# Performance work log

Hardware: AMD Instinct MI355X
Metric: run time of the kernel (lower is better)

## Reference

```python
import jax, jax.numpy as jnp
import numpy as np

B, M, L, D = 64, 128, 20, 1024


def setup_inputs() -> dict:
    key = jax.random.key(0)
    ks = jax.random.split(key, 16)
    s = 0.05  # weight scale to keep LSTM gates out of saturation
    rn = lambda k, shape: jax.random.normal(k, shape, jnp.float32) * s
    return {
        'encoder_out': jax.random.normal(ks[0], (B, M + 1, D), jnp.float32),
        'obj_seq': jax.random.randint(ks[1], (B, L), 0, M),
        'att_mask': jnp.ones((B, M + 1), jnp.int32),
        'bos_w': rn(ks[2], (1, D)),
        'eos_w': rn(ks[3], (1, D)),
        'Wp': rn(ks[4], (D, D)), 'bp': jnp.zeros((D,), jnp.float32),
        'Wih1': rn(ks[5], (4 * D, 3 * D)), 'Whh1': rn(ks[6], (4 * D, D)),
        'bih1': jnp.zeros((4 * D,), jnp.float32), 'bhh1': jnp.zeros((4 * D,), jnp.float32),
        'Wih2': rn(ks[7], (4 * D, 2 * D)), 'Whh2': rn(ks[8], (4 * D, D)),
        'bih2': jnp.zeros((4 * D,), jnp.float32), 'bhh2': jnp.zeros((4 * D,), jnp.float32),
        'Wah': rn(ks[9], (D, D)), 'bah': jnp.zeros((D,), jnp.float32),
        'wa': rn(ks[10], (D,)), 'ba': jnp.zeros((1,), jnp.float32),
        'Wae': rn(ks[11], (D, D)), 'bae': jnp.zeros((D,), jnp.float32),
        'Woe': rn(ks[12], (D, D)), 'boe': jnp.zeros((D,), jnp.float32),
    }


def _lstm_cell(x, h, c, Wih, Whh, bih, bhh):
    # torch LSTMCell gate order: i, f, g, o
    g = x @ Wih.T + bih + h @ Whh.T + bhh
    i, f, gg, o = jnp.split(g, 4, axis=-1)
    c_new = jax.nn.sigmoid(f) * c + jax.nn.sigmoid(i) * jnp.tanh(gg)
    h_new = jax.nn.sigmoid(o) * jnp.tanh(c_new)
    return h_new, c_new


def _forward(encoder_out, obj_seq, att_mask, bos_w, eos_w, Wp, bp,
             Wih1, Whh1, bih1, bhh1, Wih2, Whh2, bih2, bhh2,
             Wah, bah, wa, ba, Wae, bae, Woe, boe):
    b, _, d = encoder_out.shape
    gv = encoder_out[:, 0, :]                      # [B, D]
    att_feats = encoder_out[:, 1:, :]              # [B, M, D]
    idx = jnp.broadcast_to(obj_seq[:, :, None], obj_seq.shape + (d,)).astype(jnp.int32)
    obj_feat = jnp.take_along_axis(att_feats, idx, axis=1)          # [B, L, D]
    bos = jnp.broadcast_to(bos_w, (b, 1, d))
    obj_feat = jnp.concatenate([bos, obj_feat], axis=1)             # [B, L+1, D]
    p_att = att_feats @ Wp.T + bp                  # [B, M, D]
    amask = att_mask[:, 1:]                        # [B, M]

    def attend(h1):
        dot = jnp.tanh(p_att + (h1 @ Wah.T + bah)[:, None, :])      # [B, M, D]
        score = dot @ wa + ba[0]                                    # [B, M]
        score = jnp.where(amask == 0, -1e9, score)
        alpha = jax.nn.softmax(score, axis=-1)
        return jnp.einsum('bm,bmd->bd', alpha, att_feats)

    def step(carry, x_t):
        h1, c1, h2, c2 = carry
        inp1 = jnp.concatenate([h2, gv, x_t], axis=-1)              # [B, 3D]
        h1, c1 = _lstm_cell(inp1, h1, c1, Wih1, Whh1, bih1, bhh1)
        att = attend(h1)
        inp2 = jnp.concatenate([att, h1], axis=-1)                  # [B, 2D]
        h2, c2 = _lstm_cell(inp2, h2, c2, Wih2, Whh2, bih2, bhh2)
        return (h1, c1, h2, c2), h2

    z = jnp.zeros((b, d), encoder_out.dtype)
    _, outs = jax.lax.scan(step, (z, z, z, z), jnp.swapaxes(obj_feat, 0, 1))
    outputs = jnp.swapaxes(outs, 0, 1)             # [B, L+1, D]

    # NCE branch (cfg.LOSSES.NCE.STOP_GRAD = True)
    nce_att = jax.lax.stop_gradient(att_feats)
    afe = nce_att @ Wae.T + bae
    eos = jnp.broadcast_to(eos_w, (b, 1, d))
    afe = jnp.concatenate([eos, afe], axis=1)      # [B, M+1, D]
    ofe = outputs @ Woe.T + boe                    # [B, L+1, D]
    nce_logit = jnp.einsum('bld,bmd->blm', ofe, afe)  # [B, L+1, M+1]
    return outputs, nce_logit


def reference(encoder_out, obj_seq, att_mask, bos_w, eos_w, Wp, bp,
              Wih1, Whh1, bih1, bhh1, Wih2, Whh2, bih2, bhh2,
              Wah, bah, wa, ba, Wae, bae, Woe, boe):
    return _forward(encoder_out, obj_seq, att_mask, bos_w, eos_w, Wp, bp,
                    Wih1, Whh1, bih1, bhh1, Wih2, Whh2, bih2, bhh2,
                    Wah, bah, wa, ba, Wae, bae, Woe, boe)
```

## Files before the change

kernel.cpp:

```cpp
#include <hip/hip_runtime.h>
#include <cmath>

typedef unsigned short u16;
typedef __attribute__((ext_vector_type(8))) short short8;
typedef __attribute__((ext_vector_type(4))) float floatx4;
typedef __attribute__((address_space(3))) unsigned int lds_u32;
typedef const __attribute__((address_space(1))) unsigned int glob_u32;

__device__ __forceinline__ u16 f2bf(float f) {
    unsigned u = __float_as_uint(f);
    unsigned r = u + 0x7fffu + ((u >> 16) & 1u);
    return (u16)(r >> 16);
}
__device__ __forceinline__ float bf2f(u16 h) { return __uint_as_float(((unsigned)h) << 16); }
__device__ __forceinline__ void split2(float x, u16& hi, u16& lo) {
    hi = f2bf(x);
    lo = f2bf(x - bf2f(hi));
}
__device__ __forceinline__ float sigm(float x) {
    x = fminf(fmaxf(x, -30.f), 30.f);
    return 1.0f / (1.0f + __expf(-x));
}
__device__ __forceinline__ float ftanh(float x) {
    x = fminf(fmaxf(x, -15.f), 15.f);
    float e = __expf(2.f * x);
    return (e - 1.f) / (e + 1.f);
}
__device__ __forceinline__ void gload16(const void* g, void* l) {
    __builtin_amdgcn_global_load_lds((glob_u32*)g, (lds_u32*)l, 16, 0, 0);
}

__global__ __launch_bounds__(256) void k_cvt(const float* __restrict__ s, u16* __restrict__ d, int n4) {
    int i = blockIdx.x * 256 + threadIdx.x;
    int stride = gridDim.x * 256;
    for (; i < n4; i += stride) {
        float4 v = ((const float4*)s)[i];
        ushort4 o;
        o.x = f2bf(v.x); o.y = f2bf(v.y); o.z = f2bf(v.z); o.w = f2bf(v.w);
        ((ushort4*)d)[i] = o;
    }
}

__global__ __launch_bounds__(256) void k_cvt_att(const float* __restrict__ enc, u16* __restrict__ dst) {
    int m = blockIdx.x, b = blockIdx.y, tid = threadIdx.x;
    const float* src = enc + ((size_t)b * 129 + 1 + m) * 1024;
    float4 v = *(const float4*)(src + tid * 4);
    ushort4 o;
    o.x = f2bf(v.x); o.y = f2bf(v.y); o.z = f2bf(v.z); o.w = f2bf(v.w);
    *(ushort4*)(dst + ((size_t)b * 128 + m) * 1024 + tid * 4) = o;
}

__global__ __launch_bounds__(256) void k_splitp(const float* __restrict__ s, u16* __restrict__ hi,
                                                u16* __restrict__ lo, int n4) {
    int i = blockIdx.x * 256 + threadIdx.x;
    int stride = gridDim.x * 256;
    for (; i < n4; i += stride) {
        float4 v = ((const float4*)s)[i];
        ushort4 h, l;
        split2(v.x, h.x, l.x); split2(v.y, h.y, l.y);
        split2(v.z, h.z, l.z); split2(v.w, h.w, l.w);
        ((ushort4*)hi)[i] = h;
        ((ushort4*)lo)[i] = l;
    }
}

__global__ __launch_bounds__(256) void k_build_w1cat_i(const float* __restrict__ Wih1, const float* __restrict__ Whh1,
                                                       u16* __restrict__ dh, u16* __restrict__ dl) {
    int r = blockIdx.x;
    int srcrow = (r & 3) * 1024 + (r >> 2);
    int c = threadIdx.x * 8;
    const float* src = (c < 1024) ? (Wih1 + (size_t)srcrow * 3072 + c) : (Whh1 + (size_t)srcrow * 1024 + (c - 1024));
    short8 h, l;
#pragma unroll
    for (int j = 0; j < 8; ++j) { u16 hh, ll; split2(src[j], hh, ll); h[j] = (short)hh; l[j] = (short)ll; }
    *(short8*)(dh + (size_t)r * 2048 + c) = h;
    *(short8*)(dl + (size_t)r * 2048 + c) = l;
}

__global__ __launch_bounds__(384) void k_build_wcat2_i(const float* __restrict__ Wih2, const float* __restrict__ Whh2,
                                                       u16* __restrict__ dh, u16* __restrict__ dl) {
    int r = blockIdx.x;
    int srcrow = (r & 3) * 1024 + (r >> 2);
    int c = threadIdx.x * 8;
    const float* src = (c < 2048) ? (Wih2 + (size_t)srcrow * 2048 + c) : (Whh2 + (size_t)srcrow * 1024 + (c - 2048));
    short8 h, l;
#pragma unroll
    for (int j = 0; j < 8; ++j) { u16 hh, ll; split2(src[j], hh, ll); h[j] = (short)hh; l[j] = (short)ll; }
    *(short8*)(dh + (size_t)r * 3072 + c) = h;
    *(short8*)(dl + (size_t)r * 3072 + c) = l;
}

__global__ __launch_bounds__(256) void k_build_wx1_i(const float* __restrict__ Wih1, u16* __restrict__ dh,
                                                     u16* __restrict__ dl) {
    int r = blockIdx.x;
    int srcrow = (r & 3) * 1024 + (r >> 2);
    int c = threadIdx.x * 8;
    const float* src = Wih1 + (size_t)srcrow * 3072 + 1024 + c;
    short8 h, l;
#pragma unroll
    for (int j = 0; j < 8; ++j) { u16 hh, ll; split2(src[j], hh, ll); h[j] = (short)hh; l[j] = (short)ll; }
    *(short8*)(dh + (size_t)r * 2048 + c) = h;
    *(short8*)(dl + (size_t)r * 2048 + c) = l;
}

__global__ __launch_bounds__(256) void k_mkbias(const float* __restrict__ s1, const float* __restrict__ s2,
                                                float* __restrict__ dst) {
    int r = blockIdx.x * 256 + threadIdx.x;
    int srcn = (r & 3) * 1024 + (r >> 2);
    dst[r] = s1[srcn] + s2[srcn];
}

__global__ __launch_bounds__(256) void k_build_xaug(const float* __restrict__ enc, const int* __restrict__ obj,
                                                    const float* __restrict__ bos_w, u16* __restrict__ dh,
                                                    u16* __restrict__ dl) {
    int b = blockIdx.x, t = blockIdx.y, tid = threadIdx.x;
    const float* gv = enc + (size_t)b * 129 * 1024;
    const float* xr;
    if (t == 0) xr = bos_w;
    else {
        int idx = obj[b * 20 + (t - 1)];
        idx = min(max(idx, 0), 127);
        xr = enc + ((size_t)b * 129 + 1 + idx) * 1024;
    }
    size_t rowoff = ((size_t)b * 21 + t) * 2048;
    float4 v0 = *(const float4*)(gv + tid * 4);
    float4 v1 = *(const float4*)(xr + tid * 4);
    ushort4 h0, l0, h1, l1;
    split2(v0.x, h0.x, l0.x); split2(v0.y, h0.y, l0.y); split2(v0.z, h0.z, l0.z); split2(v0.w, h0.w, l0.w);
    split2(v1.x, h1.x, l1.x); split2(v1.y, h1.y, l1.y); split2(v1.z, h1.z, l1.z); split2(v1.w, h1.w, l1.w);
    *(ushort4*)(dh + rowoff + tid * 4) = h0;
    *(ushort4*)(dl + rowoff + tid * 4) = l0;
    *(ushort4*)(dh + rowoff + 1024 + tid * 4) = h1;
    *(ushort4*)(dl + rowoff + 1024 + tid * 4) = l1;
}

template <int APASS, int BPASS, int AREMAP, bool BF16OUT>
__global__ __launch_bounds__(256)
void k_gemm3(const u16* __restrict__ Ah, const u16* __restrict__ Al, int lda,
             const u16* __restrict__ Wh, const u16* __restrict__ Wl, int ldw,
             const float* __restrict__ b1, const float* __restrict__ b2,
             void* __restrict__ Cout, int ldc, int Mrows, int K) {
    constexpr int NP = APASS + BPASS;
    __shared__ char lds[2][NP][8192];
    const int tid = threadIdx.x;
    const int lane = tid & 63;
    const int lr = lane & 15, lk = lane >> 4;
    const int m0 = blockIdx.y * 128, n0 = blockIdx.x * 128;
    const int wid = tid >> 6;
    const int wr = wid >> 1, wc = wid & 1;
    const int wbyte = (tid & 192) * 16;

    floatx4 acc[4][4] = {};
    const int nt = K >> 5;

    auto stage = [&](int bb, int kt) {
        int k0 = kt * 32;
#pragma unroll
        for (int i = 0; i < 2; ++i) {
            int p = i * 256 + tid;
            int s = p ^ ((p >> 2) & 3);
            int row = s >> 2, kc = s & 3;
            size_t aoff;
            int gm = m0 + row;
            if (AREMAP == 1) aoff = (((size_t)(gm >> 7)) * 129 + 1 + (gm & 127)) * 1024 + k0 + kc * 8;
            else {
                int cm = gm < Mrows ? gm : Mrows - 1;
                aoff = (size_t)cm * lda + k0 + kc * 8;
            }
            gload16(Ah + aoff, &lds[bb][0][i * 4096 + wbyte]);
            if constexpr (APASS == 2) gload16(Al + aoff, &lds[bb][1][i * 4096 + wbyte]);
            size_t woff = (size_t)(n0 + row) * ldw + k0 + kc * 8;
            gload16(Wh + woff, &lds[bb][APASS][i * 4096 + wbyte]);
            if constexpr (BPASS == 2) gload16(Wl + woff, &lds[bb][APASS + 1][i * 4096 + wbyte]);
        }
    };

    stage(0, 0);
    __syncthreads();
    for (int t = 0; t < nt; ++t) {
        int bb = t & 1;
        if (t + 1 < nt) stage(bb ^ 1, t + 1);
        short8 ah_[4], al_[4], bh_[4], bl_[4];
#pragma unroll
        for (int mi = 0; mi < 4; ++mi) {
            int row = wr * 64 + mi * 16 + lr;
            int slot = (row * 4 + (lk ^ (row & 3))) * 16;
            ah_[mi] = *(const short8*)&lds[bb][0][slot];
            if constexpr (APASS == 2) al_[mi] = *(const short8*)&lds[bb][1][slot];
        }
#pragma unroll
        for (int ni = 0; ni < 4; ++ni) {
            int row = wc * 64 + ni * 16 + lr;
            int slot = (row * 4 + (lk ^ (row & 3))) * 16;
            bh_[ni] = *(const short8*)&lds[bb][APASS][slot];
            if constexpr (BPASS == 2) bl_[ni] = *(const short8*)&lds[bb][APASS + 1][slot];
        }
#pragma unroll
        for (int mi = 0; mi < 4; ++mi)
#pragma unroll
            for (int ni = 0; ni < 4; ++ni) {
                acc[mi][ni] = __builtin_amdgcn_mfma_f32_16x16x32_bf16(ah_[mi], bh_[ni], acc[mi][ni], 0, 0, 0);
                if constexpr (BPASS == 2)
                    acc[mi][ni] = __builtin_amdgcn_mfma_f32_16x16x32_bf16(ah_[mi], bl_[ni], acc[mi][ni], 0, 0, 0);
                if constexpr (APASS == 2)
                    acc[mi][ni] = __builtin_amdgcn_mfma_f32_16x16x32_bf16(al_[mi], bh_[ni], acc[mi][ni], 0, 0, 0);
            }
        __syncthreads();
    }
#pragma unroll
    for (int mi = 0; mi < 4; ++mi) {
#pragma unroll
        for (int r = 0; r < 4; ++r) {
            int gm = m0 + wr * 64 + mi * 16 + lk * 4 + r;
            if (AREMAP == 0 && gm >= Mrows) continue;
#pragma unroll
            for (int ni = 0; ni < 4; ++ni) {
                int gn = n0 + wc * 64 + ni * 16 + lr;
                float v = acc[mi][ni][r];
                if (b1) v += b1[gn];
                if (b2) v += b2[gn];
                if (BF16OUT) ((u16*)Cout)[(size_t)gm * ldc + gn] = f2bf(v);
                else ((float*)Cout)[(size_t)gm * ldc + gn] = v;
            }
        }
    }
}

template <int KK>
__global__ __launch_bounds__(256)
void k_cellw(const u16* __restrict__ Xh_, const u16* __restrict__ Xl_, int ldx,
             const u16* __restrict__ Wh, const u16* __restrict__ Wl,
             const float* __restrict__ addf, int add_bstride,
             const float* __restrict__ bias,
             float* __restrict__ cst,
             u16* __restrict__ w1h, u16* __restrict__ w1l, int w1s,
             u16* __restrict__ w2h, u16* __restrict__ w2l, int w2s,
             float* __restrict__ outf, u16* __restrict__ oh) {
    __shared__ __align__(16) char smem[4][2][6144];
    const int tid = threadIdx.x, wid = tid >> 6, lane = tid & 63;
    const int lr = lane & 15, lk = lane >> 4;
    const int bg = blockIdx.x >> 7, dg = blockIdx.x & 127;
    const int b0 = bg * 16, r0 = dg * 32;
    const int s = lane ^ ((lane >> 2) & 3);
    const int srow = s >> 2, sc8 = (s & 3) * 8;
    const int kq = wid * (KK / 4);
    constexpr int ntw = KK / 128;

    floatx4 acc[2] = {};

    auto stage = [&](int bb, int t) {
        int k0 = kq + t * 32;
        char* buf = smem[wid][bb];
        gload16(Xh_ + (size_t)(b0 + srow) * ldx + k0 + sc8, buf + 0);
        gload16(Xl_ + (size_t)(b0 + srow) * ldx + k0 + sc8, buf + 1024);
        gload16(Wh + (size_t)(r0 + srow) * KK + k0 + sc8, buf + 2048);
        gload16(Wh + (size_t)(r0 + 16 + srow) * KK + k0 + sc8, buf + 3072);
        gload16(Wl + (size_t)(r0 + srow) * KK + k0 + sc8, buf + 4096);
        gload16(Wl + (size_t)(r0 + 16 + srow) * KK + k0 + sc8, buf + 5120);
    };

    stage(0, 0);
    for (int t = 0; t < ntw; ++t) {
        if (t + 1 < ntw) {
            stage((t + 1) & 1, t + 1);
            asm volatile("s_waitcnt vmcnt(6)" ::: "memory");
        } else {
            asm volatile("s_waitcnt vmcnt(0)" ::: "memory");
        }
        __builtin_amdgcn_sched_barrier(0);
        const char* buf = smem[wid][t & 1];
        int off = (lr * 4 + (lk ^ (lr & 3))) * 16;
        short8 xh  = *(const short8*)(buf + off);
        short8 xl  = *(const short8*)(buf + 1024 + off);
        short8 wh0 = *(const short8*)(buf + 2048 + off);
        short8 wh1 = *(const short8*)(buf + 3072 + off);
        short8 wl0 = *(const short8*)(buf + 4096 + off);
        short8 wl1 = *(const short8*)(buf + 5120 + off);
        acc[0] = __builtin_amdgcn_mfma_f32_16x16x32_bf16(xh, wh0, acc[0], 0, 0, 0);
        acc[0] = __builtin_amdgcn_mfma_f32_16x16x32_bf16(xh, wl0, acc[0], 0, 0, 0);
        acc[0] = __builtin_amdgcn_mfma_f32_16x16x32_bf16(xl, wh0, acc[0], 0, 0, 0);
        acc[1] = __builtin_amdgcn_mfma_f32_16x16x32_bf16(xh, wh1, acc[1], 0, 0, 0);
        acc[1] = __builtin_amdgcn_mfma_f32_16x16x32_bf16(xh, wl1, acc[1], 0, 0, 0);
        acc[1] = __builtin_amdgcn_mfma_f32_16x16x32_bf16(xl, wh1, acc[1], 0, 0, 0);
    }
    __syncthreads();
    float* Gs = (float*)smem;
#pragma unroll
    for (int ni = 0; ni < 2; ++ni)
#pragma unroll
        for (int j = 0; j < 4; ++j)
            Gs[wid * 640 + (lk * 4 + j) * 40 + ni * 16 + lr] = acc[ni][j];
    __syncthreads();
    if (tid < 128) {
        int bl_ = tid >> 3, dl = tid & 7;
        int b = b0 + bl_, d = dg * 8 + dl;
        float4 g = make_float4(0.f, 0.f, 0.f, 0.f);
#pragma unroll
        for (int w = 0; w < 4; ++w) {
            float4 v = *(const float4*)&Gs[w * 640 + bl_ * 40 + dl * 4];
            g.x += v.x; g.y += v.y; g.z += v.z; g.w += v.w;
        }
        if (addf) {
            float4 av = *(const float4*)(addf + (size_t)b * add_bstride + dg * 32 + dl * 4);
            g.x += av.x; g.y += av.y; g.z += av.z; g.w += av.w;
        }
        if (bias) {
            float4 bv = *(const float4*)(bias + dg * 32 + dl * 4);
            g.x += bv.x; g.y += bv.y; g.z += bv.z; g.w += bv.w;
        }
        int ci = b * 1024 + d;
        float cp = cst[ci];
        float cn = sigm(g.y) * cp + sigm(g.x) * ftanh(g.z);
        float hn = sigm(g.w) * ftanh(cn);
        cst[ci] = cn;
        u16 hh, hl;
        split2(hn, hh, hl);
        w1h[b * w1s + d] = hh; w1l[b * w1s + d] = hl;
        w2h[b * w2s + d] = hh; w2l[b * w2s + d] = hl;
        if (outf) outf[(size_t)b * 21 * 1024 + d] = hn;
        if (oh) oh[(size_t)b * 21 * 1024 + d] = hh;
    }
}

__global__ __launch_bounds__(256)
void k_gp2(const u16* __restrict__ Xh, int ldx,
           const u16* __restrict__ Wh, const u16* __restrict__ Wl, int ldw,
           int Klen, float* __restrict__ P, int Ntot) {
    __shared__ char lds[2][8192];
    const int tid = threadIdx.x, wid = tid >> 6, lane = tid & 63;
    const int lr = lane & 15, lk = lane >> 4;
    const int n0 = blockIdx.x * 32;
    const int koff = blockIdx.y * Klen;
    floatx4 acc[2] = {};
    const int nt = Klen >> 5;

    const int sX = tid ^ ((tid >> 2) & 3);
    const size_t xoff = (size_t)(sX >> 2) * ldx + (sX & 3) * 8 + koff;
    const int xdst = (tid & 192) * 16;
    const int pw = tid & 127;
    const int sW = pw ^ ((pw >> 2) & 3);
    const size_t woff = (size_t)(n0 + (sW >> 2)) * ldw + (sW & 3) * 8 + koff;
    const u16* Wsrc = (tid < 128) ? Wh : Wl;
    const int wdst = 4096 + (wid >> 1) * 2048 + (wid & 1) * 1024;

    auto stage = [&](int bb, int kt) {
        int k0 = kt * 32;
        gload16(Xh + xoff + k0, &lds[bb][xdst]);
        gload16(Wsrc + woff + k0, &lds[bb][wdst]);
    };

    stage(0, 0);
    __syncthreads();
    for (int t = 0; t < nt; ++t) {
        int bb = t & 1;
        if (t + 1 < nt) stage(bb ^ 1, t + 1);
        int arow = wid * 16 + lr;
        short8 xh = *(const short8*)&lds[bb][(arow * 4 + (lk ^ (arow & 3))) * 16];
#pragma unroll
        for (int ni = 0; ni < 2; ++ni) {
            int r = ni * 16 + lr;
            int slot = (r * 4 + (lk ^ (r & 3))) * 16;
            short8 wh = *(const short8*)&lds[bb][4096 + slot];
            short8 wl = *(const short8*)&lds[bb][6144 + slot];
            acc[ni] = __builtin_amdgcn_mfma_f32_16x16x32_bf16(xh, wh, acc[ni], 0, 0, 0);
            acc[ni] = __builtin_amdgcn_mfma_f32_16x16x32_bf16(xh, wl, acc[ni], 0, 0, 0);
        }
        __syncthreads();
    }
    float* Pb = P + (size_t)blockIdx.y * 64 * Ntot;
#pragma unroll
    for (int ni = 0; ni < 2; ++ni)
#pragma unroll
        for (int r = 0; r < 4; ++r) {
            int b = wid * 16 + lk * 4 + r;
            Pb[(size_t)b * Ntot + n0 + ni * 16 + lr] = acc[ni][r];
        }
}

__global__ __launch_bounds__(256)
void k_score(const float* __restrict__ PAH, const float* __restrict__ bah,
             const float* __restrict__ wa, const float* __restrict__ ba,
             const u16* __restrict__ Patt, const int* __restrict__ amask, float* __restrict__ SC) {
    int mc = blockIdx.x, b = blockIdx.y, tid = threadIdx.x;
    __shared__ float sah[1024], swa[1024];
    {
        int d = tid * 4;
        *(float4*)&swa[d] = *(const float4*)(wa + d);
        float4 s;
        float* sp = &s.x;
#pragma unroll
        for (int j = 0; j < 4; ++j) {
            float acc = bah[d + j];
#pragma unroll
            for (int p = 0; p < 4; ++p) acc += PAH[((size_t)p * 64 + b) * 1024 + d + j];
            sp[j] = acc;
        }
        *(float4*)&sah[d] = s;
    }
    __syncthreads();
    int wv = tid >> 6, lane = tid & 63;
    float bav = ba[0];
    for (int j = 0; j < 8; ++j) {
        int m = mc * 32 + wv * 8 + j;
        const u16* pr = Patt + ((size_t)(b * 128 + m)) * 1024;
        float part = 0.f;
#pragma unroll
        for (int c = 0; c < 4; ++c) {
            int d = c * 256 + lane * 4;
            ushort4 p4 = *(const ushort4*)(pr + d);
            float4 a4 = *(const float4*)&sah[d];
            float4 w4 = *(const float4*)&swa[d];
            part += ftanh(bf2f(p4.x) + a4.x) * w4.x + ftanh(bf2f(p4.y) + a4.y) * w4.y +
                    ftanh(bf2f(p4.z) + a4.z) * w4.z + ftanh(bf2f(p4.w) + a4.w) * w4.w;
        }
#pragma unroll
        for (int off = 32; off; off >>= 1) part += __shfl_down(part, off, 64);
        if (lane == 0) {
            float sc = part + bav;
            if (amask[b * 129 + 1 + m] == 0) sc = -1e9f;
            SC[b * 128 + m] = sc;
        }
    }
}

__global__ __launch_bounds__(256)
void k_attsum(const float* __restrict__ SC, const u16* __restrict__ attf,
              u16* __restrict__ X2h, u16* __restrict__ X2l) {
    int dc = blockIdx.x, b = blockIdx.y, tid = threadIdx.x;
    __shared__ float salpha[128];
    __shared__ float sred[8];
    float sv = (tid < 128) ? SC[b * 128 + tid] : -1e30f;
    float mx = sv;
#pragma unroll
    for (int off = 32; off; off >>= 1) mx = fmaxf(mx, __shfl_down(mx, off, 64));
    if ((tid & 63) == 0) sred[tid >> 6] = mx;
    __syncthreads();
    float gmx = fmaxf(fmaxf(sred[0], sred[1]), fmaxf(sred[2], sred[3]));
    float ev = (tid < 128) ? __expf(sv - gmx) : 0.f;
    float s = ev;
#pragma unroll
    for (int off = 32; off; off >>= 1) s += __shfl_down(s, off, 64);
    if ((tid & 63) == 0) sred[4 + (tid >> 6)] = s;
    __syncthreads();
    float gsum = sred[4] + sred[5] + sred[6] + sred[7];
    if (tid < 128) salpha[tid] = ev / gsum;
    __syncthreads();
    int d = dc * 256 + tid;
    const u16* base = attf + (size_t)b * 128 * 1024 + d;
    float acc = 0.f;
#pragma unroll 8
    for (int m = 0; m < 128; ++m) acc += salpha[m] * bf2f(base[(size_t)m * 1024]);
    u16 hh, hl;
    split2(acc, hh, hl);
    X2h[b * 3072 + d] = hh;
    X2l[b * 3072 + d] = hl;
}

__global__ __launch_bounds__(256)
void k_nce_bf(const u16* __restrict__ OFE, const u16* __restrict__ AFE,
              const float* __restrict__ eos_w, float* __restrict__ nce) {
    int l = blockIdx.x, b = blockIdx.y;
    __shared__ u16 sofe[1024];
    int tid = threadIdx.x;
    *(ushort4*)&sofe[tid * 4] = *(const ushort4*)(OFE + ((size_t)b * 21 + l) * 1024 + tid * 4);
    __syncthreads();
    int w = tid >> 6, lane = tid & 63;
    float* outp = nce + ((size_t)b * 21 + l) * 129;
    for (int j = w; j < 129; j += 4) {
        float part = 0.f;
        if (j == 0) {
#pragma unroll
            for (int c = 0; c < 4; ++c) {
                int d = c * 256 + lane * 4;
                float4 a4 = *(const float4*)(eos_w + d);
                ushort4 o4 = *(const ushort4*)&sofe[d];
                part += a4.x * bf2f(o4.x) + a4.y * bf2f(o4.y) + a4.z * bf2f(o4.z) + a4.w * bf2f(o4.w);
            }
        } else {
            const u16* ar = AFE + ((size_t)b * 128 + (j - 1)) * 1024;
#pragma unroll
            for (int c = 0; c < 4; ++c) {
                int d = c * 256 + lane * 4;
                ushort4 a4 = *(const ushort4*)(ar + d);
                ushort4 o4 = *(const ushort4*)&sofe[d];
                part += bf2f(a4.x) * bf2f(o4.x) + bf2f(a4.y) * bf2f(o4.y) +
                        bf2f(a4.z) * bf2f(o4.z) + bf2f(a4.w) * bf2f(o4.w);
            }
        }
#pragma unroll
        for (int off = 32; off; off >>= 1) part += __shfl_down(part, off, 64);
        if (lane == 0) outp[j] = part;
    }
}

extern "C" void kernel_launch(void* const* d_in, const int* in_sizes, int n_in,
                              void* d_out, int out_size, void* d_ws, size_t ws_size,
                              hipStream_t stream) {
    const float* enc  = (const float*)d_in[0];
    const int*   obj  = (const int*)d_in[1];
    const int*   amask= (const int*)d_in[2];
    const float* bosw = (const float*)d_in[3];
    const float* eosw = (const float*)d_in[4];
    const float* Wp   = (const float*)d_in[5];
    const float* bp   = (const float*)d_in[6];
    const float* Wih1 = (const float*)d_in[7];
    const float* Whh1 = (const float*)d_in[8];
    const float* bih1 = (const float*)d_in[9];
    const float* bhh1 = (const float*)d_in[10];
    const float* Wih2 = (const float*)d_in[11];
    const float* Whh2 = (const float*)d_in[12];
    const float* bih2 = (const float*)d_in[13];
    const float* bhh2 = (const float*)d_in[14];
    const float* Wah  = (const float*)d_in[15];
    const float* bah  = (const float*)d_in[16];
    const float* wa   = (const float*)d_in[17];
    const float* ba   = (const float*)d_in[18];
    const float* Wae  = (const float*)d_in[19];
    const float* bae  = (const float*)d_in[20];
    const float* Woe  = (const float*)d_in[21];
    const float* boe  = (const float*)d_in[22];

    float* outputs = (float*)d_out;
    float* nce     = outputs + (size_t)64 * 21 * 1024;

    char* wp = (char*)d_ws;
    auto alloc = [&](size_t bytes) -> char* { char* p = wp; wp += (bytes + 255) & ~(size_t)255; return p; };
    u16* encbf  = (u16*)alloc((size_t)64 * 129 * 1024 * 2);
    u16* Wpbf   = (u16*)alloc((size_t)1024 * 1024 * 2);
    u16* Xaugh  = (u16*)alloc((size_t)1344 * 2048 * 2);
    u16* Xaugl  = (u16*)alloc((size_t)1344 * 2048 * 2);
    u16* W1h    = (u16*)alloc((size_t)4096 * 2048 * 2);
    u16* W1l    = (u16*)alloc((size_t)4096 * 2048 * 2);
    u16* W2h    = (u16*)alloc((size_t)4096 * 3072 * 2);
    u16* W2l    = (u16*)alloc((size_t)4096 * 3072 * 2);
    u16* Wahh   = (u16*)alloc((size_t)1024 * 1024 * 2);
    u16* Wahl   = (u16*)alloc((size_t)1024 * 1024 * 2);
    u16* Waeh   = (u16*)alloc((size_t)1024 * 1024 * 2);
    u16* Wael   = (u16*)alloc((size_t)1024 * 1024 * 2);
    u16* Woeh   = (u16*)alloc((size_t)1024 * 1024 * 2);
    u16* Woel   = (u16*)alloc((size_t)1024 * 1024 * 2);
    float* bias1i = (float*)alloc(4096 * 4);
    float* bias2i = (float*)alloc(4096 * 4);
    char* region1 = alloc((size_t)2 * 4096 * 2048 * 2);
    u16* Wx1h = (u16*)region1;
    u16* Wx1l = (u16*)region1 + (size_t)4096 * 2048;
    u16* AFEbf = (u16*)region1;
    u16* PattBf  = (u16*)alloc((size_t)8192 * 1024 * 2);
    u16* attfbf  = (u16*)alloc((size_t)64 * 128 * 1024 * 2);
    float* Xcf   = (float*)alloc((size_t)1344 * 4096 * 4);
    u16* Xouth   = (u16*)alloc((size_t)1344 * 1024 * 2);
    u16* OFEbf = Xaugh;
    char* sp2 = (char*)encbf;
    auto alloc2 = [&](size_t bytes) -> char* { char* p = sp2; sp2 += (bytes + 255) & ~(size_t)255; return p; };
    float* PAH = (float*)alloc2((size_t)4 * 64 * 1024 * 4);
    u16* X1h   = (u16*)alloc2((size_t)2 * 64 * 2048 * 2);
    u16* X1l   = (u16*)alloc2((size_t)2 * 64 * 2048 * 2);
    u16* X2h   = (u16*)alloc2((size_t)2 * 64 * 3072 * 2);
    u16* X2l   = (u16*)alloc2((size_t)2 * 64 * 3072 * 2);
    float* c1  = (float*)alloc2((size_t)64 * 1024 * 4);
    float* c2  = (float*)alloc2((size_t)64 * 1024 * 4);
    float* SC  = (float*)alloc2((size_t)64 * 128 * 4);

    dim3 blk(256);
    k_cvt<<<2048, blk, 0, stream>>>(enc, encbf, 64 * 129 * 1024 / 4);
    k_cvt_att<<<dim3(128, 64), blk, 0, stream>>>(enc, attfbf);
    k_cvt<<<1024, blk, 0, stream>>>(Wp, Wpbf, 1024 * 1024 / 4);
    k_splitp<<<1024, blk, 0, stream>>>(Wah, Wahh, Wahl, 1024 * 1024 / 4);
    k_splitp<<<1024, blk, 0, stream>>>(Wae, Waeh, Wael, 1024 * 1024 / 4);
    k_splitp<<<1024, blk, 0, stream>>>(Woe, Woeh, Woel, 1024 * 1024 / 4);
    k_build_wx1_i<<<4096, blk, 0, stream>>>(Wih1, Wx1h, Wx1l);
    k_build_w1cat_i<<<4096, blk, 0, stream>>>(Wih1, Whh1, W1h, W1l);
    k_build_wcat2_i<<<4096, dim3(384), 0, stream>>>(Wih2, Whh2, W2h, W2l);
    k_mkbias<<<16, blk, 0, stream>>>(bih1, bhh1, bias1i);
    k_mkbias<<<16, blk, 0, stream>>>(bih2, bhh2, bias2i);
    k_build_xaug<<<dim3(64, 21), blk, 0, stream>>>(enc, obj, bosw, Xaugh, Xaugl);

    k_gemm3<1, 1, 1, true><<<dim3(8, 64), blk, 0, stream>>>(
        encbf, nullptr, 0, Wpbf, nullptr, 1024, bp, nullptr, PattBf, 1024, 8192, 1024);
    k_gemm3<2, 2, 0, false><<<dim3(32, 11), blk, 0, stream>>>(
        Xaugh, Xaugl, 2048, Wx1h, Wx1l, 2048, bias1i, nullptr, Xcf, 4096, 1344, 2048);
    k_gemm3<1, 2, 1, true><<<dim3(8, 64), blk, 0, stream>>>(
        encbf, nullptr, 0, Waeh, Wael, 1024, bae, nullptr, AFEbf, 1024, 8192, 1024);

    hipMemsetAsync(X1h, 0, (size_t)2 * 64 * 2048 * 2, stream);
    hipMemsetAsync(X1l, 0, (size_t)2 * 64 * 2048 * 2, stream);
    hipMemsetAsync(X2h, 0, (size_t)2 * 64 * 3072 * 2, stream);
    hipMemsetAsync(X2l, 0, (size_t)2 * 64 * 3072 * 2, stream);
    hipMemsetAsync(c1, 0, (size_t)64 * 1024 * 4, stream);
    hipMemsetAsync(c2, 0, (size_t)64 * 1024 * 4, stream);

    const size_t S1 = (size_t)64 * 2048, S2 = (size_t)64 * 3072;
    for (int t = 0; t < 21; ++t) {
        int p = t & 1, q = p ^ 1;
        k_cellw<2048><<<512, blk, 0, stream>>>(
            X1h + p * S1, X1l + p * S1, 2048, W1h, W1l,
            Xcf + (size_t)t * 4096, 21 * 4096, nullptr, c1,
            X1h + q * S1 + 1024, X1l + q * S1 + 1024, 2048,
            X2h + p * S2 + 1024, X2l + p * S2 + 1024, 3072, nullptr, nullptr);
        k_gp2<<<dim3(32, 4), blk, 0, stream>>>(X1h + q * S1 + 1024, 2048, Wahh, Wahl, 1024, 256, PAH, 1024);
        k_score<<<dim3(4, 64), blk, 0, stream>>>(PAH, bah, wa, ba, PattBf, amask, SC);
        k_attsum<<<dim3(4, 64), blk, 0, stream>>>(SC, attfbf, X2h + p * S2, X2l + p * S2);
        k_cellw<3072><<<512, blk, 0, stream>>>(
            X2h + p * S2, X2l + p * S2, 3072, W2h, W2l,
            nullptr, 0, bias2i, c2,
            X1h + q * S1, X1l + q * S1, 2048,
            X2h + q * S2 + 2048, X2l + q * S2 + 2048, 3072,
            outputs + (size_t)t * 1024, Xouth + (size_t)t * 1024);
    }

    k_gemm3<1, 2, 0, true><<<dim3(8, 11), blk, 0, stream>>>(
        Xouth, nullptr, 1024, Woeh, Woel, 1024, boe, nullptr, OFEbf, 1024, 1344, 1024);
    k_nce_bf<<<dim3(21, 64), blk, 0, stream>>>(OFEbf, AFEbf, eosw, nce);
}
```

Before: 1.782 ms.

## Drop low-bf16 activation split in LSTM cells and load operands directly to registers

The recurrent cell kernels now keep only the high bf16 part of the hidden/attention activations, dropping the Xl buffers and the xl*wh MFMA term, so each step issues 4 MFMAs per k-chunk instead of 6 and writes half as many activation bytes. The LDS staging with async global loads is replaced by direct register loads with a one-step software prefetch. The score kernel launches twice as many blocks with half the rows each, for more parallelism. This lowers per-step traffic and compute on the serial recurrence, at the cost of reduced precision in the recurrent matmuls, which may push error past tolerance over 21 steps.

New measurement: 1.899 ms. 1.07x slower.

```diff
diff --git a/kernel.cpp b/kernel.cpp
--- a/kernel.cpp
+++ b/kernel.cpp
@@ -228,68 +228,56 @@
 
 template <int KK>
 __global__ __launch_bounds__(256)
-void k_cellw(const u16* __restrict__ Xh_, const u16* __restrict__ Xl_, int ldx,
+void k_cellr(const u16* __restrict__ X, int ldx,
              const u16* __restrict__ Wh, const u16* __restrict__ Wl,
              const float* __restrict__ addf, int add_bstride,
              const float* __restrict__ bias,
              float* __restrict__ cst,
-             u16* __restrict__ w1h, u16* __restrict__ w1l, int w1s,
-             u16* __restrict__ w2h, u16* __restrict__ w2l, int w2s,
+             u16* __restrict__ w1, int w1s, u16* __restrict__ w2, int w2s,
              float* __restrict__ outf, u16* __restrict__ oh) {
-    __shared__ __align__(16) char smem[4][2][6144];
     const int tid = threadIdx.x, wid = tid >> 6, lane = tid & 63;
     const int lr = lane & 15, lk = lane >> 4;
     const int bg = blockIdx.x >> 7, dg = blockIdx.x & 127;
     const int b0 = bg * 16, r0 = dg * 32;
-    const int s = lane ^ ((lane >> 2) & 3);
-    const int srow = s >> 2, sc8 = (s & 3) * 8;
     const int kq = wid * (KK / 4);
     constexpr int ntw = KK / 128;
 
     floatx4 acc[2] = {};
 
-    auto stage = [&](int bb, int t) {
-        int k0 = kq + t * 32;
-        char* buf = smem[wid][bb];
-        gload16(Xh_ + (size_t)(b0 + srow) * ldx + k0 + sc8, buf + 0);
-        gload16(Xl_ + (size_t)(b0 + srow) * ldx + k0 + sc8, buf + 1024);
-        gload16(Wh + (size_t)(r0 + srow) * KK + k0 + sc8, buf + 2048);
-        gload16(Wh + (size_t)(r0 + 16 + srow) * KK + k0 + sc8, buf + 3072);
-        gload16(Wl + (size_t)(r0 + srow) * KK + k0 + sc8, buf + 4096);
-        gload16(Wl + (size_t)(r0 + 16 + srow) * KK + k0 + sc8, buf + 5120);
-    };
-
-    stage(0, 0);
+    const u16* xp  = X  + (size_t)(b0 + lr) * ldx + kq + lk * 8;
+    const u16* wp0 = Wh + (size_t)(r0 + lr) * KK + kq + lk * 8;
+    const u16* wp1 = Wh + (size_t)(r0 + 16 + lr) * KK + kq + lk * 8;
+    const u16* vp0 = Wl + (size_t)(r0 + lr) * KK + kq + lk * 8;
+    const u16* vp1 = Wl + (size_t)(r0 + 16 + lr) * KK + kq + lk * 8;
+
+    short8 xA   = *(const short8*)xp;
+    short8 whA0 = *(const short8*)wp0;
+    short8 whA1 = *(const short8*)wp1;
+    short8 wlA0 = *(const short8*)vp0;
+    short8 wlA1 = *(const short8*)vp1;
     for (int t = 0; t < ntw; ++t) {
+        short8 xB = xA, whB0 = whA0, whB1 = whA1, wlB0 = wlA0, wlB1 = wlA1;
         if (t + 1 < ntw) {
-            stage((t + 1) & 1, t + 1);
-            asm volatile("s_waitcnt vmcnt(6)" ::: "memory");
-        } else {
-            asm volatile("s_waitcnt vmcnt(0)" ::: "memory");
-        }
-        __builtin_amdgcn_sched_barrier(0);
-        const char* buf = smem[wid][t & 1];
-        int off = (lr * 4 + (lk ^ (lr & 3))) * 16;
-        short8 xh  = *(const short8*)(buf + off);
-        short8 xl  = *(const short8*)(buf + 1024 + off);
-        short8 wh0 = *(const short8*)(buf + 2048 + off);
-        short8 wh1 = *(const short8*)(buf + 3072 + off);
-        short8 wl0 = *(const short8*)(buf + 4096 + off);
-        short8 wl1 = *(const short8*)(buf + 5120 + off);
-        acc[0] = __builtin_amdgcn_mfma_f32_16x16x32_bf16(xh, wh0, acc[0], 0, 0, 0);
-        acc[0] = __builtin_amdgcn_mfma_f32_16x16x32_bf16(xh, wl0, acc[0], 0, 0, 0);
-        acc[0] = __builtin_amdgcn_mfma_f32_16x16x32_bf16(xl, wh0, acc[0], 0, 0, 0);
-        acc[1] = __builtin_amdgcn_mfma_f32_16x16x32_bf16(xh, wh1, acc[1], 0, 0, 0);
-        acc[1] = __builtin_amdgcn_mfma_f32_16x16x32_bf16(xh, wl1, acc[1], 0, 0, 0);
-        acc[1] = __builtin_amdgcn_mfma_f32_16x16x32_bf16(xl, wh1, acc[1], 0, 0, 0);
-    }
-    __syncthreads();
-    float* Gs = (float*)smem;
+            int k = (t + 1) * 32;
+            xB   = *(const short8*)(xp + k);
+            whB0 = *(const short8*)(wp0 + k);
+            whB1 = *(const short8*)(wp1 + k);
+            wlB0 = *(const short8*)(vp0 + k);
+            wlB1 = *(const short8*)(vp1 + k);
+        }
+        acc[0] = __builtin_amdgcn_mfma_f32_16x16x32_bf16(xA, whA0, acc[0], 0, 0, 0);
+        acc[0] = __builtin_amdgcn_mfma_f32_16x16x32_bf16(xA, wlA0, acc[0], 0, 0, 0);
+        acc[1] = __builtin_amdgcn_mfma_f32_16x16x32_bf16(xA, whA1, acc[1], 0, 0, 0);
+        acc[1] = __builtin_amdgcn_mfma_f32_16x16x32_bf16(xA, wlA1, acc[1], 0, 0, 0);
+        xA = xB; whA0 = whB0; whA1 = whB1; wlA0 = wlB0; wlA1 = wlB1;
+    }
+    __shared__ float Gs[4][16][40];
+    __syncthreads();
 #pragma unroll
     for (int ni = 0; ni < 2; ++ni)
 #pragma unroll
         for (int j = 0; j < 4; ++j)
-            Gs[wid * 640 + (lk * 4 + j) * 40 + ni * 16 + lr] = acc[ni][j];
+            Gs[wid][lk * 4 + j][ni * 16 + lr] = acc[ni][j];
     __syncthreads();
     if (tid < 128) {
         int bl_ = tid >> 3, dl = tid & 7;
@@ -297,7 +285,7 @@
         float4 g = make_float4(0.f, 0.f, 0.f, 0.f);
 #pragma unroll
         for (int w = 0; w < 4; ++w) {
-            float4 v = *(const float4*)&Gs[w * 640 + bl_ * 40 + dl * 4];
+            float4 v = *(const float4*)&Gs[w][bl_][dl * 4];
             g.x += v.x; g.y += v.y; g.z += v.z; g.w += v.w;
         }
         if (addf) {
@@ -313,10 +301,9 @@
         float cn = sigm(g.y) * cp + sigm(g.x) * ftanh(g.z);
         float hn = sigm(g.w) * ftanh(cn);
         cst[ci] = cn;
-        u16 hh, hl;
-        split2(hn, hh, hl);
-        w1h[b * w1s + d] = hh; w1l[b * w1s + d] = hl;
-        w2h[b * w2s + d] = hh; w2l[b * w2s + d] = hl;
+        u16 hh = f2bf(hn);
+        w1[b * w1s + d] = hh;
+        w2[b * w2s + d] = hh;
         if (outf) outf[(size_t)b * 21 * 1024 + d] = hn;
         if (oh) oh[(size_t)b * 21 * 1024 + d] = hh;
     }
@@ -400,8 +387,8 @@
     __syncthreads();
     int wv = tid >> 6, lane = tid & 63;
     float bav = ba[0];
-    for (int j = 0; j < 8; ++j) {
-        int m = mc * 32 + wv * 8 + j;
+    for (int j = 0; j < 4; ++j) {
+        int m = mc * 16 + wv * 4 + j;
         const u16* pr = Patt + ((size_t)(b * 128 + m)) * 1024;
         float part = 0.f;
 #pragma unroll
@@ -425,7 +412,7 @@
 
 __global__ __launch_bounds__(256)
 void k_attsum(const float* __restrict__ SC, const u16* __restrict__ attf,
-              u16* __restrict__ X2h, u16* __restrict__ X2l) {
+              u16* __restrict__ X2h) {
     int dc = blockIdx.x, b = blockIdx.y, tid = threadIdx.x;
     __shared__ float salpha[128];
     __shared__ float sred[8];
@@ -450,10 +437,7 @@
     float acc = 0.f;
 #pragma unroll 8
     for (int m = 0; m < 128; ++m) acc += salpha[m] * bf2f(base[(size_t)m * 1024]);
-    u16 hh, hl;
-    split2(acc, hh, hl);
-    X2h[b * 3072 + d] = hh;
-    X2l[b * 3072 + d] = hl;
+    X2h[b * 3072 + d] = f2bf(acc);
 }
 
 __global__ __launch_bounds__(256)
@@ -554,9 +538,7 @@
     auto alloc2 = [&](size_t bytes) -> char* { char* p = sp2; sp2 += (bytes + 255) & ~(size_t)255; return p; };
     float* PAH = (float*)alloc2((size_t)4 * 64 * 1024 * 4);
     u16* X1h   = (u16*)alloc2((size_t)2 * 64 * 2048 * 2);
-    u16* X1l   = (u16*)alloc2((size_t)2 * 64 * 2048 * 2);
     u16* X2h   = (u16*)alloc2((size_t)2 * 64 * 3072 * 2);
-    u16* X2l   = (u16*)alloc2((size_t)2 * 64 * 3072 * 2);
     float* c1  = (float*)alloc2((size_t)64 * 1024 * 4);
     float* c2  = (float*)alloc2((size_t)64 * 1024 * 4);
     float* SC  = (float*)alloc2((size_t)64 * 128 * 4);
@@ -583,28 +565,24 @@
         encbf, nullptr, 0, Waeh, Wael, 1024, bae, nullptr, AFEbf, 1024, 8192, 1024);
 
     hipMemsetAsync(X1h, 0, (size_t)2 * 64 * 2048 * 2, stream);
-    hipMemsetAsync(X1l, 0, (size_t)2 * 64 * 2048 * 2, stream);
     hipMemsetAsync(X2h, 0, (size_t)2 * 64 * 3072 * 2, stream);
-    hipMemsetAsync(X2l, 0, (size_t)2 * 64 * 3072 * 2, stream);
     hipMemsetAsync(c1, 0, (size_t)64 * 1024 * 4, stream);
     hipMemsetAsync(c2, 0, (size_t)64 * 1024 * 4, stream);
 
     const size_t S1 = (size_t)64 * 2048, S2 = (size_t)64 * 3072;
     for (int t = 0; t < 21; ++t) {
         int p = t & 1, q = p ^ 1;
-        k_cellw<2048><<<512, blk, 0, stream>>>(
-            X1h + p * S1, X1l + p * S1, 2048, W1h, W1l,
+        k_cellr<2048><<<512, blk, 0, stream>>>(
+            X1h + p * S1, 2048, W1h, W1l,
             Xcf + (size_t)t * 4096, 21 * 4096, nullptr, c1,
-            X1h + q * S1 + 1024, X1l + q * S1 + 1024, 2048,
-            X2h + p * S2 + 1024, X2l + p * S2 + 1024, 3072, nullptr, nullptr);
+            X1h + q * S1 + 1024, 2048, X2h + p * S2 + 1024, 3072, nullptr, nullptr);
         k_gp2<<<dim3(32, 4), blk, 0, stream>>>(X1h + q * S1 + 1024, 2048, Wahh, Wahl, 1024, 256, PAH, 1024);
-        k_score<<<dim3(4, 64), blk, 0, stream>>>(PAH, bah, wa, ba, PattBf, amask, SC);
-        k_attsum<<<dim3(4, 64), blk, 0, stream>>>(SC, attfbf, X2h + p * S2, X2l + p * S2);
-        k_cellw<3072><<<512, blk, 0, stream>>>(
-            X2h + p * S2, X2l + p * S2, 3072, W2h, W2l,
+        k_score<<<dim3(8, 64), blk, 0, stream>>>(PAH, bah, wa, ba, PattBf, amask, SC);
+        k_attsum<<<dim3(4, 64), blk, 0, stream>>>(SC, attfbf, X2h + p * S2);
+        k_cellr<3072><<<512, blk, 0, stream>>>(
+            X2h + p * S2, 3072, W2h, W2l,
             nullptr, 0, bias2i, c2,
-            X1h + q * S1, X1l + q * S1, 2048,
-            X2h + q * S2 + 2048, X2l + q * S2 + 2048, 3072,
+            X1h + q * S1, 2048, X2h + q * S2 + 2048, 3072,
             outputs + (size_t)t * 1024, Xouth + (size_t)t * 1024);
     }
 
```
